# Kernel tuning notes

Measured on AMD Instinct MI355X. Metric: run time of the kernel, lower is better.

The kernel has to match this reference:

```python
import jax, jax.numpy as jnp
import numpy as np

D_MODEL = 1024
NUM_HEADS = 16
D_K = D_MODEL // NUM_HEADS
SIM_THRESH = 0.7


def setup_inputs() -> dict:
    key = jax.random.key(0)
    ks = jax.random.split(key, 7)
    bs, seq = 2, 2048
    scale = 1.0 / np.sqrt(D_MODEL)
    x = jax.random.normal(ks[0], (bs, seq, D_MODEL), dtype=jnp.float32)
    Wq = jax.random.normal(ks[1], (D_MODEL, D_MODEL), dtype=jnp.float32) * scale
    Wk = jax.random.normal(ks[2], (D_MODEL, D_MODEL), dtype=jnp.float32) * scale
    Wv = jax.random.normal(ks[3], (D_MODEL, D_MODEL), dtype=jnp.float32) * scale
    bq = jax.random.normal(ks[4], (D_MODEL,), dtype=jnp.float32) * scale
    bk = jax.random.normal(ks[5], (D_MODEL,), dtype=jnp.float32) * scale
    bv = jax.random.normal(ks[6], (D_MODEL,), dtype=jnp.float32) * scale
    return {"x": x, "Wq": Wq, "bq": bq, "Wk": Wk, "bk": bk, "Wv": Wv, "bv": bv}


def reference(x, Wq, bq, Wk, bk, Wv, bv):
    bs, seq, d_model = x.shape
    # dynamic structural mask: cosine similarity > 0.7, shared across heads
    norm_x = x / jnp.maximum(jnp.linalg.norm(x, axis=-1, keepdims=True), 1e-12)
    sim = jnp.einsum('bsd,btd->bst', norm_x, norm_x)          # [B,S,S]
    mask = (sim > SIM_THRESH)[:, None, :, :]                  # [B,1,S,S]

    def proj(W, b):
        y = x @ W.T + b                                        # [B,S,D]
        return y.reshape(bs, seq, NUM_HEADS, D_K).transpose(0, 2, 1, 3)  # [B,H,S,dk]

    q = proj(Wq, bq)
    k = proj(Wk, bk)
    v = proj(Wv, bv)

    scores = jnp.einsum('bhsd,bhtd->bhst', q, k) / jnp.sqrt(jnp.float32(D_K))
    scores = jnp.where(mask, scores, -jnp.inf)
    attn = jax.nn.softmax(scores, axis=-1)                     # diag always unmasked
    return jnp.einsum('bhst,bhtd->bhsd', attn, v)              # [B,H,S,dk]
```

## Files before the change

kernel.cpp:

```cpp
#include <hip/hip_runtime.h>
#include <stdint.h>
#include <math.h>

#define D_MODEL 1024
#define NUM_HEADS 16
#define D_K 64
#define SEQ 2048
#define BATCH 2
#define SIM_THRESH 0.7f
#define ITHRESH 11290

#define TS 128
#define NITV (D_MODEL / 32)
#define NITS (D_MODEL / 64)

#define NROWS (BATCH * SEQ)
#define VP_BLOCKS ((NROWS / TS) * (D_MODEL / TS))
#define SIM_ROWB (SEQ / TS)
#define SIM_TRI (SIM_ROWB * (SIM_ROWB + 1) / 2)
#define SIM_BLOCKS (SIM_TRI * BATCH)
#define GRID (VP_BLOCKS + SIM_BLOCKS)
#define VP_PER_XCD (VP_BLOCKS / 8)
#define SIM_PER_XCD (SIM_BLOCKS / 8)

#define TILE_B 8192

typedef __attribute__((ext_vector_type(8))) short bf16x8;
typedef __attribute__((ext_vector_type(4))) float f32x4;
typedef __attribute__((ext_vector_type(4))) int i32x4;

static __device__ __forceinline__ unsigned short f2bf(float f) {
    unsigned int u = __float_as_uint(f);
    unsigned int r = (u + 0x7FFF + ((u >> 16) & 1)) >> 16;
    return (unsigned short)r;
}
static __device__ __forceinline__ float bf2f(unsigned short u) {
    return __uint_as_float(((unsigned int)u) << 16);
}

__global__ __launch_bounds__(256) void k_prep(const float* __restrict__ x,
                                              const float* __restrict__ Wv,
                                              unsigned short* __restrict__ xn,
                                              unsigned short* __restrict__ Wvb,
                                              char* __restrict__ xq,
                                              float* __restrict__ norms,
                                              int* __restrict__ cnt) {
    int bid = blockIdx.x, tid = threadIdx.x;
    if (bid < NROWS) {
        const float4* xr = (const float4*)(x + (size_t)bid * D_MODEL);
        float4 vv = xr[tid];
        float ss = vv.x * vv.x + vv.y * vv.y + vv.z * vv.z + vv.w * vv.w;
        for (int off = 32; off > 0; off >>= 1) ss += __shfl_down(ss, off, 64);
        __shared__ float wsum[4];
        int lane = tid & 63, wv = tid >> 6;
        if (lane == 0) wsum[wv] = ss;
        __syncthreads();
        float nrm = sqrtf(wsum[0] + wsum[1] + wsum[2] + wsum[3]);
        float inv = 1.0f / fmaxf(nrm, 1e-12f);
        float n0 = vv.x * inv, n1 = vv.y * inv, n2 = vv.z * inv, n3 = vv.w * inv;
        ushort4 o;
        o.x = f2bf(n0); o.y = f2bf(n1); o.z = f2bf(n2); o.w = f2bf(n3);
        *(ushort4*)(xn + (size_t)bid * D_MODEL + tid * 4) = o;
        char4 q;
        q.x = (char)__float2int_rn(n0 * 127.f);
        q.y = (char)__float2int_rn(n1 * 127.f);
        q.z = (char)__float2int_rn(n2 * 127.f);
        q.w = (char)__float2int_rn(n3 * 127.f);
        *(char4*)(xq + (size_t)bid * D_MODEL + tid * 4) = q;
        if (tid == 0) { norms[bid] = nrm; cnt[bid] = 0; }
    } else {
        size_t i = (size_t)(bid - NROWS) * 256 + tid;
        float4 w = ((const float4*)Wv)[i];
        ushort4 o;
        o.x = f2bf(w.x); o.y = f2bf(w.y); o.z = f2bf(w.z); o.w = f2bf(w.w);
        *(ushort4*)(Wvb + i * 4) = o;
    }
}

static __device__ __forceinline__ void stage8k(const char* __restrict__ gsrc,
                                               int rowStrideB, int kByte,
                                               char* ldsDst, int tid) {
#pragma unroll
    for (int i = 0; i < 2; ++i) {
        int c   = i * 256 + tid;
        int row = c >> 2;
        int ch  = c & 3;
        const char* ga = gsrc + (size_t)row * rowStrideB + kByte + ch * 16;
        __builtin_amdgcn_global_load_lds(
            (const __attribute__((address_space(1))) unsigned int*)ga,
            (__attribute__((address_space(3))) unsigned int*)(ldsDst + c * 16),
            16, 0, 0);
    }
}

__global__ __launch_bounds__(256, 2) void k_main(const unsigned short* __restrict__ xn,
                                                 const unsigned short* __restrict__ Wvb,
                                                 const char* __restrict__ xq,
                                                 const float* __restrict__ bv,
                                                 const float* __restrict__ norms,
                                                 int* __restrict__ cnt,
                                                 float* __restrict__ out) {
    __shared__ char As[4 * TILE_B];
    __shared__ char Bs[4 * TILE_B];
    int bid0 = blockIdx.x;
    int xcd = bid0 & 7, l = bid0 >> 3;
    int tid = threadIdx.x;
    int lane = tid & 63, wave = tid >> 6;
    int wm = wave & 1, wn = wave >> 1;
    int lrow = lane & 15, quad = lane >> 4;

    bool isV = (l < VP_PER_XCD);

    int aoffB[4], boffB[4];
#pragma unroll
    for (int i = 0; i < 4; ++i) {
        aoffB[i] = (wm * 64 + i * 16 + lrow) * 64 + quad * 16;
        boffB[i] = (wn * 64 + i * 16 + lrow) * 64 + quad * 16;
    }

    if (isV) {
        int bid = xcd * VP_PER_XCD + l;
        int rowBase = (bid >> 3) * TS;
        int colBase = (bid & 7) * TS;
        const char* Asrc = (const char*)(xn + (size_t)rowBase * D_MODEL);
        const char* Bsrc = (const char*)(Wvb + (size_t)colBase * D_MODEL);

        f32x4 acc[4][4] = {};
        stage8k(Asrc, 2048, 0, As, tid);
        stage8k(Bsrc, 2048, 0, Bs, tid);
        stage8k(Asrc, 2048, 64, As + TILE_B, tid);
        stage8k(Bsrc, 2048, 64, Bs + TILE_B, tid);
        __syncthreads();
        for (int t = 0; t < NITV / 2; ++t) {
            if (t + 1 < NITV / 2) {
                int s0 = (2 * t + 2) & 3, s1 = (2 * t + 3) & 3;
                stage8k(Asrc, 2048, (2 * t + 2) * 64, As + s0 * TILE_B, tid);
                stage8k(Bsrc, 2048, (2 * t + 2) * 64, Bs + s0 * TILE_B, tid);
                stage8k(Asrc, 2048, (2 * t + 3) * 64, As + s1 * TILE_B, tid);
                stage8k(Bsrc, 2048, (2 * t + 3) * 64, Bs + s1 * TILE_B, tid);
            }
#pragma unroll
            for (int sub = 0; sub < 2; ++sub) {
                const char* Ac = As + ((2 * t + sub) & 3) * TILE_B;
                const char* Bc = Bs + ((2 * t + sub) & 3) * TILE_B;
                bf16x8 av[4], bw[4];
#pragma unroll
                for (int i = 0; i < 4; ++i) av[i] = *(const bf16x8*)(Ac + aoffB[i]);
#pragma unroll
                for (int i = 0; i < 4; ++i) bw[i] = *(const bf16x8*)(Bc + boffB[i]);
#pragma unroll
                for (int mt = 0; mt < 4; ++mt)
#pragma unroll
                    for (int nt = 0; nt < 4; ++nt)
                        acc[mt][nt] = __builtin_amdgcn_mfma_f32_16x16x32_bf16(av[mt], bw[nt], acc[mt][nt], 0, 0, 0);
            }
            __syncthreads();
        }
#pragma unroll
        for (int nt = 0; nt < 4; ++nt) {
            int n = colBase + wn * 64 + nt * 16 + lrow;
            float bn = bv[n];
            int h = n >> 6, j = n & 63;
#pragma unroll
            for (int mt = 0; mt < 4; ++mt) {
#pragma unroll
                for (int r = 0; r < 4; ++r) {
                    int m = rowBase + wm * 64 + mt * 16 + quad * 4 + r;
                    float val = acc[mt][nt][r] * norms[m] + bn;
                    int bb = m >> 11, s = m & (SEQ - 1);
                    out[(((size_t)(bb * NUM_HEADS + h)) * SEQ + s) * D_K + j] = val;
                }
            }
        }
    } else {
        int sidx = xcd * SIM_PER_XCD + (l - VP_PER_XCD);
        int b = (sidx >= SIM_TRI) ? 1 : 0;
        int r0 = sidx - b * SIM_TRI;
        int bi = 0;
        while (r0 >= SIM_ROWB - bi) { r0 -= SIM_ROWB - bi; ++bi; }
        int bj = bi + r0;
        int rowBase = bi * TS;
        int colBase = bj * TS;
        const char* base = xq + (size_t)b * SEQ * D_MODEL;
        const char* Asrc = base + (size_t)rowBase * D_MODEL;
        const char* Bsrc = base + (size_t)colBase * D_MODEL;
        bool diag = (bi == bj);

        i32x4 acc[4][4] = {};
        stage8k(Asrc, 1024, 0, As, tid);
        stage8k(Asrc, 1024, 64, As + TILE_B, tid);
        if (!diag) {
            stage8k(Bsrc, 1024, 0, Bs, tid);
            stage8k(Bsrc, 1024, 64, Bs + TILE_B, tid);
        }
        __syncthreads();
        for (int t = 0; t < NITS / 2; ++t) {
            if (t + 1 < NITS / 2) {
                int s0 = (2 * t + 2) & 3, s1 = (2 * t + 3) & 3;
                stage8k(Asrc, 1024, (2 * t + 2) * 64, As + s0 * TILE_B, tid);
                stage8k(Asrc, 1024, (2 * t + 3) * 64, As + s1 * TILE_B, tid);
                if (!diag) {
                    stage8k(Bsrc, 1024, (2 * t + 2) * 64, Bs + s0 * TILE_B, tid);
                    stage8k(Bsrc, 1024, (2 * t + 3) * 64, Bs + s1 * TILE_B, tid);
                }
            }
#pragma unroll
            for (int sub = 0; sub < 2; ++sub) {
                const char* Ac = As + ((2 * t + sub) & 3) * TILE_B;
                const char* Bc = (diag ? As : Bs) + ((2 * t + sub) & 3) * TILE_B;
                i32x4 av[4], bw[4];
#pragma unroll
                for (int i = 0; i < 4; ++i) av[i] = *(const i32x4*)(Ac + aoffB[i]);
#pragma unroll
                for (int i = 0; i < 4; ++i) bw[i] = *(const i32x4*)(Bc + boffB[i]);
#pragma unroll
                for (int mt = 0; mt < 4; ++mt)
#pragma unroll
                    for (int nt = 0; nt < 4; ++nt)
                        acc[mt][nt] = __builtin_amdgcn_mfma_i32_16x16x64_i8(av[mt], bw[nt], acc[mt][nt], 0, 0, 0);
            }
            __syncthreads();
        }
        int* cb = cnt + b * SEQ;
#pragma unroll
        for (int nt = 0; nt < 4; ++nt) {
            int n = colBase + wn * 64 + nt * 16 + lrow;
#pragma unroll
            for (int mt = 0; mt < 4; ++mt) {
#pragma unroll
                for (int r = 0; r < 4; ++r) {
                    int m = rowBase + wm * 64 + mt * 16 + quad * 4 + r;
                    if (acc[mt][nt][r] > ITHRESH) {
                        atomicAdd(&cb[m], 1);
                        if (!diag) atomicAdd(&cb[n], 1);
                    }
                }
            }
        }
    }
}

__global__ __launch_bounds__(256) void k_fix(
    const float* __restrict__ x,
    const float* __restrict__ Wq, const float* __restrict__ bq,
    const float* __restrict__ Wk, const float* __restrict__ bk,
    const float* __restrict__ Wv, const float* __restrict__ bv,
    const unsigned short* __restrict__ xn,
    const int* __restrict__ cnt,
    float* __restrict__ out)
{
    int tid = threadIdx.x;
    int rowBase = blockIdx.x * 256;

    __shared__ int list[256];
    __shared__ int nlist;
    if (tid == 0) nlist = 0;
    __syncthreads();
    int grow = rowBase + tid;
    if (cnt[grow] != 1) { int p = atomicAdd(&nlist, 1); list[p] = grow; }
    __syncthreads();
    int nfix = nlist;
    if (nfix == 0) return;

    __shared__ uint8_t mrow[SEQ];
    __shared__ float q_row[D_MODEL];
    __shared__ float k_row[D_MODEL];
    __shared__ float v_row[D_MODEL];
    __shared__ float accO[D_MODEL];
    __shared__ float m_h[NUM_HEADS], l_h[NUM_HEADS], alpha_h[NUM_HEADS], p_h[NUM_HEADS];

    for (int li = 0; li < nfix; ++li) {
        int row = list[li];
        int b = row >> 11, s = row & (SEQ - 1);

        const unsigned short* xs = xn + (size_t)row * D_MODEL;
        for (int t = tid; t < SEQ; t += 256) {
            const unsigned short* xt = xn + ((size_t)b * SEQ + t) * D_MODEL;
            float d = 0.f;
            for (int k = 0; k < D_MODEL; ++k) d += bf2f(xs[k]) * bf2f(xt[k]);
            mrow[t] = (d > SIM_THRESH) ? 1 : 0;
        }

        const float* xrow = x + (size_t)row * D_MODEL;
        for (int c = tid; c < D_MODEL; c += 256) {
            const float* w = Wq + (size_t)c * D_MODEL;
            float acc = bq[c];
            for (int d = 0; d < D_MODEL; ++d) acc += xrow[d] * w[d];
            q_row[c] = acc;
            accO[c] = 0.f;
        }
        if (tid < NUM_HEADS) { m_h[tid] = -INFINITY; l_h[tid] = 0.f; }
        __syncthreads();

        for (int t = 0; t < SEQ; ++t) {
            if (!mrow[t]) continue;
            const float* xt = x + ((size_t)b * SEQ + t) * D_MODEL;
            for (int c = tid; c < D_MODEL; c += 256) {
                const float* wk = Wk + (size_t)c * D_MODEL;
                const float* wv = Wv + (size_t)c * D_MODEL;
                float ak = bk[c], av = bv[c];
                for (int d = 0; d < D_MODEL; ++d) {
                    float xv = xt[d];
                    ak += xv * wk[d];
                    av += xv * wv[d];
                }
                k_row[c] = ak;
                v_row[c] = av;
            }
            __syncthreads();
            if (tid < NUM_HEADS) {
                float sc = 0.f;
                for (int j = 0; j < D_K; ++j) sc += q_row[tid * D_K + j] * k_row[tid * D_K + j];
                sc *= 0.125f;
                float mnew = fmaxf(m_h[tid], sc);
                float alpha = expf(m_h[tid] - mnew);
                float p = expf(sc - mnew);
                l_h[tid] = l_h[tid] * alpha + p;
                m_h[tid] = mnew;
                alpha_h[tid] = alpha;
                p_h[tid] = p;
            }
            __syncthreads();
            for (int c = tid; c < D_MODEL; c += 256) {
                int h = c >> 6;
                accO[c] = accO[c] * alpha_h[h] + p_h[h] * v_row[c];
            }
            __syncthreads();
        }
        for (int c = tid; c < D_MODEL; c += 256) {
            int h = c >> 6, j = c & 63;
            out[(((size_t)(b * NUM_HEADS + h)) * SEQ + s) * D_K + j] = accO[c] / l_h[h];
        }
        __syncthreads();
    }
}

extern "C" void kernel_launch(void* const* d_in, const int* in_sizes, int n_in,
                              void* d_out, int out_size, void* d_ws, size_t ws_size,
                              hipStream_t stream) {
    const float* x  = (const float*)d_in[0];
    const float* Wq = (const float*)d_in[1];
    const float* bq = (const float*)d_in[2];
    const float* Wk = (const float*)d_in[3];
    const float* bk = (const float*)d_in[4];
    const float* Wv = (const float*)d_in[5];
    const float* bv = (const float*)d_in[6];
    float* out = (float*)d_out;

    unsigned short* xn  = (unsigned short*)d_ws;
    unsigned short* Wvb = xn + (size_t)NROWS * D_MODEL;
    char* xq     = (char*)(Wvb + (size_t)D_MODEL * D_MODEL);
    float* norms = (float*)(xq + (size_t)NROWS * D_MODEL);
    int* cnt     = (int*)(norms + NROWS);

    k_prep<<<NROWS + D_MODEL * D_MODEL / 1024, 256, 0, stream>>>(x, Wv, xn, Wvb, xq, norms, cnt);

    k_main<<<GRID, 256, 0, stream>>>(xn, Wvb, xq, bv, norms, cnt, out);

    k_fix<<<NROWS / 256, 256, 0, stream>>>(x, Wq, bq, Wk, bk, Wv, bv, xn, cnt, out);
}
```

Before: 112.0 us.

## Pipeline GEMM K-loop per stage with partial vmcnt waits and raw barriers

Both the V-projection and similarity GEMM loops move from processing two K-stages per iteration with full __syncthreads to one stage per iteration. Each iteration issues the loads for stage t+2 into a 4-slot ring, waits only until the older stage's loads have landed (partial s_waitcnt vmcnt), then uses a raw s_barrier. The goal is to keep two stages of global-to-LDS loads in flight while computing and to avoid draining every outstanding load at each barrier. It relies on stage8k issuing exactly the assumed number of vector memory ops per call (likely direct-to-LDS loads). If that count is wrong, or the compiler reorders loads, the waits become unsafe.

```diff
diff --git a/kernel.cpp b/kernel.cpp
--- a/kernel.cpp
+++ b/kernel.cpp
@@ -28,6 +28,12 @@
 typedef __attribute__((ext_vector_type(8))) short bf16x8;
 typedef __attribute__((ext_vector_type(4))) float f32x4;
 typedef __attribute__((ext_vector_type(4))) int i32x4;
+
+#define VM_WAIT(N) asm volatile("s_waitcnt vmcnt(" #N ")" ::: "memory")
+static __device__ __forceinline__ void barrier_raw() {
+    __builtin_amdgcn_s_barrier();
+    asm volatile("" ::: "memory");
+}
 
 static __device__ __forceinline__ unsigned short f2bf(float f) {
     unsigned int u = __float_as_uint(f);
@@ -130,31 +136,30 @@
         stage8k(Bsrc, 2048, 0, Bs, tid);
         stage8k(Asrc, 2048, 64, As + TILE_B, tid);
         stage8k(Bsrc, 2048, 64, Bs + TILE_B, tid);
-        __syncthreads();
-        for (int t = 0; t < NITV / 2; ++t) {
-            if (t + 1 < NITV / 2) {
-                int s0 = (2 * t + 2) & 3, s1 = (2 * t + 3) & 3;
-                stage8k(Asrc, 2048, (2 * t + 2) * 64, As + s0 * TILE_B, tid);
-                stage8k(Bsrc, 2048, (2 * t + 2) * 64, Bs + s0 * TILE_B, tid);
-                stage8k(Asrc, 2048, (2 * t + 3) * 64, As + s1 * TILE_B, tid);
-                stage8k(Bsrc, 2048, (2 * t + 3) * 64, Bs + s1 * TILE_B, tid);
-            }
-#pragma unroll
-            for (int sub = 0; sub < 2; ++sub) {
-                const char* Ac = As + ((2 * t + sub) & 3) * TILE_B;
-                const char* Bc = Bs + ((2 * t + sub) & 3) * TILE_B;
-                bf16x8 av[4], bw[4];
-#pragma unroll
-                for (int i = 0; i < 4; ++i) av[i] = *(const bf16x8*)(Ac + aoffB[i]);
-#pragma unroll
-                for (int i = 0; i < 4; ++i) bw[i] = *(const bf16x8*)(Bc + boffB[i]);
-#pragma unroll
-                for (int mt = 0; mt < 4; ++mt)
-#pragma unroll
-                    for (int nt = 0; nt < 4; ++nt)
-                        acc[mt][nt] = __builtin_amdgcn_mfma_f32_16x16x32_bf16(av[mt], bw[nt], acc[mt][nt], 0, 0, 0);
-            }
-            __syncthreads();
+        for (int t = 0; t < NITV; ++t) {
+            if (t + 2 < NITV) {
+                int sb = (t + 2) & 3;
+                stage8k(Asrc, 2048, (t + 2) * 64, As + sb * TILE_B, tid);
+                stage8k(Bsrc, 2048, (t + 2) * 64, Bs + sb * TILE_B, tid);
+                VM_WAIT(8);
+            } else if (t + 2 == NITV) {
+                VM_WAIT(4);
+            } else {
+                VM_WAIT(0);
+            }
+            barrier_raw();
+            const char* Ac = As + (t & 3) * TILE_B;
+            const char* Bc = Bs + (t & 3) * TILE_B;
+            bf16x8 av[4], bw[4];
+#pragma unroll
+            for (int i = 0; i < 4; ++i) av[i] = *(const bf16x8*)(Ac + aoffB[i]);
+#pragma unroll
+            for (int i = 0; i < 4; ++i) bw[i] = *(const bf16x8*)(Bc + boffB[i]);
+#pragma unroll
+            for (int mt = 0; mt < 4; ++mt)
+#pragma unroll
+                for (int nt = 0; nt < 4; ++nt)
+                    acc[mt][nt] = __builtin_amdgcn_mfma_f32_16x16x32_bf16(av[mt], bw[nt], acc[mt][nt], 0, 0, 0);
         }
 #pragma unroll
         for (int nt = 0; nt < 4; ++nt) {
@@ -193,33 +198,34 @@
             stage8k(Bsrc, 1024, 0, Bs, tid);
             stage8k(Bsrc, 1024, 64, Bs + TILE_B, tid);
         }
-        __syncthreads();
-        for (int t = 0; t < NITS / 2; ++t) {
-            if (t + 1 < NITS / 2) {
-                int s0 = (2 * t + 2) & 3, s1 = (2 * t + 3) & 3;
-                stage8k(Asrc, 1024, (2 * t + 2) * 64, As + s0 * TILE_B, tid);
-                stage8k(Asrc, 1024, (2 * t + 3) * 64, As + s1 * TILE_B, tid);
+        for (int t = 0; t < NITS; ++t) {
+            if (t + 2 < NITS) {
+                int sb = (t + 2) & 3;
+                stage8k(Asrc, 1024, (t + 2) * 64, As + sb * TILE_B, tid);
                 if (!diag) {
-                    stage8k(Bsrc, 1024, (2 * t + 2) * 64, Bs + s0 * TILE_B, tid);
-                    stage8k(Bsrc, 1024, (2 * t + 3) * 64, Bs + s1 * TILE_B, tid);
+                    stage8k(Bsrc, 1024, (t + 2) * 64, Bs + sb * TILE_B, tid);
+                    VM_WAIT(8);
+                } else {
+                    VM_WAIT(4);
                 }
-            }
-#pragma unroll
-            for (int sub = 0; sub < 2; ++sub) {
-                const char* Ac = As + ((2 * t + sub) & 3) * TILE_B;
-                const char* Bc = (diag ? As : Bs) + ((2 * t + sub) & 3) * TILE_B;
-                i32x4 av[4], bw[4];
-#pragma unroll
-                for (int i = 0; i < 4; ++i) av[i] = *(const i32x4*)(Ac + aoffB[i]);
-#pragma unroll
-                for (int i = 0; i < 4; ++i) bw[i] = *(const i32x4*)(Bc + boffB[i]);
-#pragma unroll
-                for (int mt = 0; mt < 4; ++mt)
-#pragma unroll
-                    for (int nt = 0; nt < 4; ++nt)
-                        acc[mt][nt] = __builtin_amdgcn_mfma_i32_16x16x64_i8(av[mt], bw[nt], acc[mt][nt], 0, 0, 0);
-            }
-            __syncthreads();
+            } else if (t + 2 == NITS) {
+                if (!diag) { VM_WAIT(4); } else { VM_WAIT(2); }
+            } else {
+                VM_WAIT(0);
+            }
+            barrier_raw();
+            const char* Ac = As + (t & 3) * TILE_B;
+            const char* Bc = (diag ? As : Bs) + (t & 3) * TILE_B;
+            i32x4 av[4], bw[4];
+#pragma unroll
+            for (int i = 0; i < 4; ++i) av[i] = *(const i32x4*)(Ac + aoffB[i]);
+#pragma unroll
+            for (int i = 0; i < 4; ++i) bw[i] = *(const i32x4*)(Bc + boffB[i]);
+#pragma unroll
+            for (int mt = 0; mt < 4; ++mt)
+#pragma unroll
+                for (int nt = 0; nt < 4; ++nt)
+                    acc[mt][nt] = __builtin_amdgcn_mfma_i32_16x16x64_i8(av[mt], bw[nt], acc[mt][nt], 0, 0, 0);
         }
         int* cb = cnt + b * SEQ;
 #pragma unroll
```

Result: no change. 112.6 us (+0.5%).
